# Kernel optimization log

Measured on AMD Instinct MI355X. Metric: run time of the kernel, lower is better.

The kernel has to match this reference:

```python
import jax, jax.numpy as jnp
import numpy as np

IN_FEATURES = 512
OUT_FEATURES = 512
B_EXP = 2.0
EPS = 1e-12  # torch F.normalize eps


def setup_inputs() -> dict:
    key = jax.random.key(0)
    kz, kw = jax.random.split(key)
    z = jax.random.normal(kz, (100000, IN_FEATURES), dtype=jnp.float32)
    weight = jax.random.normal(kw, (OUT_FEATURES, IN_FEATURES), dtype=jnp.float32) * (1.0 / np.sqrt(IN_FEATURES))
    return {"z": z, "weight": weight}


def reference(z, weight):
    # lin = z @ W^T : [N, out]
    lin = jnp.einsum('ni,oi->no', z, weight)
    # row-wise L2 normalize (torch F.normalize: x / max(||x||, eps))
    z_norm = z / jnp.maximum(jnp.linalg.norm(z, axis=1, keepdims=True), EPS)
    w_norm = weight / jnp.maximum(jnp.linalg.norm(weight, axis=1, keepdims=True), EPS)
    cos = jnp.einsum('ni,oi->no', z_norm, w_norm)
    scale = jnp.abs(cos) ** (B_EXP - 1.0)
    return lin * scale
```

## Files before the change

kernel.cpp:

```cpp
#include <hip/hip_runtime.h>
#include <hip/hip_bf16.h>
#include <stdint.h>


constexpr int KDIM = 512;
constexpr int NDIM = 512;

typedef __attribute__((ext_vector_type(8))) short bf16x8;
typedef __attribute__((ext_vector_type(4))) float f32x4;
typedef __attribute__((ext_vector_type(4))) uint32_t u32x4;

__device__ __forceinline__ uint32_t pk_bf16(float a, float b) {
  __hip_bfloat162 h = __float22bfloat162_rn(make_float2(a, b));
  union { __hip_bfloat162 h2; uint32_t u; } c;
  c.h2 = h;
  return c.u;
}

__device__ __forceinline__ void gload_lds16(const void* g, void* lds) {
  __builtin_amdgcn_global_load_lds(
      (const __attribute__((address_space(1))) uint32_t*)(uintptr_t)g,
      (__attribute__((address_space(3))) uint32_t*)(uintptr_t)lds,
      16, 0, 0);
}

__global__ __launch_bounds__(128) void prep_w(const float* __restrict__ w,
                                              unsigned short* __restrict__ wb,
                                              float* __restrict__ cninv) {
  const int row = blockIdx.x;
  const int t   = threadIdx.x;
  const float* gp = w + (size_t)row * KDIM + t * 4;
  f32x4 v = *(const f32x4*)gp;
  float s = v.x * v.x + v.y * v.y + v.z * v.z + v.w * v.w;

  uint2 p;
  p.x = pk_bf16(v.x, v.y);
  p.y = pk_bf16(v.z, v.w);
  *(uint2*)(wb + (size_t)row * KDIM + t * 4) = p;

  #pragma unroll
  for (int off = 32; off > 0; off >>= 1) s += __shfl_down(s, off, 64);
  __shared__ float red[2];
  if ((t & 63) == 0) red[t >> 6] = s;
  __syncthreads();
  if (t == 0) cninv[row] = 1.0f / fmaxf(sqrtf(red[0] + red[1]), 1e-12f);
}

__global__ __launch_bounds__(256) void gemm_bcos(const float* __restrict__ z,
                                                 const unsigned short* __restrict__ wb,
                                                 const float* __restrict__ cninv,
                                                 float* __restrict__ out, int M) {
  __shared__ unsigned short As[128 * 64];
  __shared__ unsigned short Bs[128 * 64];
  __shared__ float rowsq[128];
  __shared__ float rinv[128];

  const int t    = threadIdx.x;
  const int nb   = blockIdx.x;
  const int mb   = blockIdx.y;
  const int w    = t >> 6;
  const int lane = t & 63;
  const int lrow = lane & 15;
  const int quad = lane >> 4;
  const int wm   = (w & 1) * 64;
  const int wn   = (w >> 1) * 64;

  if (t < 128) rowsq[t] = 0.0f;

  f32x4 acc[4][4];
  #pragma unroll
  for (int i = 0; i < 4; ++i)
    #pragma unroll
    for (int j = 0; j < 4; ++j) acc[i][j] = (f32x4)0.0f;

  int rr[4];
  size_t gbase[4];
  #pragma unroll
  for (int i = 0; i < 4; ++i) {
    int gidx = t + 256 * i;
    rr[i] = gidx >> 3;
    int g = gidx & 7;
    int grow = mb * 128 + rr[i];
    if (grow >= M) grow = M - 1;
    gbase[i] = (size_t)grow * KDIM + g * 8;
  }

  float sq[4] = {0.f, 0.f, 0.f, 0.f};

  for (int kk = 0; kk < 8; ++kk) {
    const int kbase = kk * 64;
    __syncthreads();

    #pragma unroll
    for (int i = 0; i < 4; ++i) {
      int cidx = t + 256 * i;
      int r = cidx >> 3, c = cidx & 7;
      gload_lds16(wb + ((size_t)(nb * 128 + r) * KDIM + kbase + c * 8), &Bs[cidx * 8]);
    }

    #pragma unroll
    for (int i = 0; i < 4; ++i) {
      const float* gp = z + gbase[i] + kbase;
      f32x4 v0 = *(const f32x4*)gp;
      f32x4 v1 = *(const f32x4*)(gp + 4);
      sq[i] += v0.x * v0.x + v0.y * v0.y + v0.z * v0.z + v0.w * v0.w +
               v1.x * v1.x + v1.y * v1.y + v1.z * v1.z + v1.w * v1.w;
      u32x4 p;
      p.x = pk_bf16(v0.x, v0.y);
      p.y = pk_bf16(v0.z, v0.w);
      p.z = pk_bf16(v1.x, v1.y);
      p.w = pk_bf16(v1.z, v1.w);
      *(u32x4*)&As[(t + 256 * i) * 8] = p;
    }

    __syncthreads();

    #pragma unroll
    for (int ks = 0; ks < 2; ++ks) {
      const int k0 = ks * 32 + quad * 8;
      bf16x8 a[4], b[4];
      #pragma unroll
      for (int x = 0; x < 4; ++x) {
        a[x] = *(const bf16x8*)&As[(wm + x * 16 + lrow) * 64 + k0];
        b[x] = *(const bf16x8*)&Bs[(wn + x * 16 + lrow) * 64 + k0];
      }
      #pragma unroll
      for (int mt = 0; mt < 4; ++mt)
        #pragma unroll
        for (int nt = 0; nt < 4; ++nt)
          acc[mt][nt] = __builtin_amdgcn_mfma_f32_16x16x32_bf16(a[mt], b[nt], acc[mt][nt], 0, 0, 0);
    }
  }

  #pragma unroll
  for (int i = 0; i < 4; ++i) atomicAdd(&rowsq[rr[i]], sq[i]);
  __syncthreads();
  if (t < 128) rinv[t] = 1.0f / fmaxf(sqrtf(rowsq[t]), 1e-12f);
  __syncthreads();

  #pragma unroll
  for (int nt = 0; nt < 4; ++nt) {
    const int colg = nb * 128 + wn + nt * 16 + lrow;
    const float cv = cninv[colg];
    #pragma unroll
    for (int mt = 0; mt < 4; ++mt) {
      const int lrm = wm + mt * 16 + quad * 4;
      #pragma unroll
      for (int i = 0; i < 4; ++i) {
        const int rowg = mb * 128 + lrm + i;
        if (rowg < M) {
          const float v = acc[mt][nt][i];
          out[(size_t)rowg * NDIM + colg] = v * fabsf(v) * rinv[lrm + i] * cv;
        }
      }
    }
  }
}

extern "C" void kernel_launch(void* const* d_in, const int* in_sizes, int n_in,
                              void* d_out, int out_size, void* d_ws, size_t ws_size,
                              hipStream_t stream) {
  const float* z = (const float*)d_in[0];
  const float* w = (const float*)d_in[1];
  float* out = (float*)d_out;
  const int M = in_sizes[0] / KDIM;

  unsigned short* wb = (unsigned short*)d_ws;
  float* cninv = (float*)((char*)d_ws + (size_t)NDIM * KDIM * 2);

  prep_w<<<dim3(NDIM), dim3(128), 0, stream>>>(w, wb, cninv);

  dim3 grid(NDIM / 128, (M + 127) / 128);
  gemm_bcos<<<grid, dim3(256), 0, stream>>>(z, wb, cninv, out, M);
}
```

Measured before the change: 489.3 us.

## Restructure GEMM so each block owns full output rows with resident z tile

Each 512-thread block now loads a 64-row slab of z once, converts it to bf16 into an XOR-swizzled LDS tile covering the full K, and computes the row norms up front. Every wave then covers 64 output columns across all 512 columns, reading bf16 weights straight from global/L2 with no LDS staging and no per-K-step barriers. This removes the previous 4x re-read and re-conversion of z across column blocks. It also adds nontemporal loads and stores for streaming data. The cost is more L2 traffic for the weights and a 64KB LDS footprint that limits occupancy.

```diff
diff --git a/kernel.cpp b/kernel.cpp
--- a/kernel.cpp
+++ b/kernel.cpp
@@ -8,20 +8,12 @@
 
 typedef __attribute__((ext_vector_type(8))) short bf16x8;
 typedef __attribute__((ext_vector_type(4))) float f32x4;
-typedef __attribute__((ext_vector_type(4))) uint32_t u32x4;
 
 __device__ __forceinline__ uint32_t pk_bf16(float a, float b) {
   __hip_bfloat162 h = __float22bfloat162_rn(make_float2(a, b));
   union { __hip_bfloat162 h2; uint32_t u; } c;
   c.h2 = h;
   return c.u;
-}
-
-__device__ __forceinline__ void gload_lds16(const void* g, void* lds) {
-  __builtin_amdgcn_global_load_lds(
-      (const __attribute__((address_space(1))) uint32_t*)(uintptr_t)g,
-      (__attribute__((address_space(3))) uint32_t*)(uintptr_t)lds,
-      16, 0, 0);
 }
 
 __global__ __launch_bounds__(128) void prep_w(const float* __restrict__ w,
@@ -46,26 +38,46 @@
   if (t == 0) cninv[row] = 1.0f / fmaxf(sqrtf(red[0] + red[1]), 1e-12f);
 }
 
-__global__ __launch_bounds__(256) void gemm_bcos(const float* __restrict__ z,
-                                                 const unsigned short* __restrict__ wb,
-                                                 const float* __restrict__ cninv,
-                                                 float* __restrict__ out, int M) {
-  __shared__ unsigned short As[128 * 64];
-  __shared__ unsigned short Bs[128 * 64];
-  __shared__ float rowsq[128];
-  __shared__ float rinv[128];
+__global__ __launch_bounds__(512, 4) void gemm_bcos(const float* __restrict__ z,
+                                                    const unsigned short* __restrict__ wb,
+                                                    const float* __restrict__ cninv,
+                                                    float* __restrict__ out, int M) {
+  __shared__ unsigned short As[64 * 512];
+  __shared__ float rowsq[64];
+  __shared__ float rinv[64];
 
   const int t    = threadIdx.x;
-  const int nb   = blockIdx.x;
-  const int mb   = blockIdx.y;
   const int w    = t >> 6;
   const int lane = t & 63;
   const int lrow = lane & 15;
   const int quad = lane >> 4;
-  const int wm   = (w & 1) * 64;
-  const int wn   = (w >> 1) * 64;
+  const int mb   = blockIdx.x;
+  const int wn   = w * 64;
 
-  if (t < 128) rowsq[t] = 0.0f;
+  #pragma unroll
+  for (int rr = 0; rr < 8; ++rr) {
+    const int rl = w * 8 + rr;
+    int rg = mb * 64 + rl;
+    if (rg >= M) rg = M - 1;
+    const float* zp = z + (size_t)rg * KDIM;
+    float s = 0.0f;
+    #pragma unroll
+    for (int j = 0; j < 2; ++j) {
+      f32x4 v = __builtin_nontemporal_load((const f32x4*)(zp + j * 256 + lane * 4));
+      s += v.x * v.x + v.y * v.y + v.z * v.z + v.w * v.w;
+      uint2 p;
+      p.x = pk_bf16(v.x, v.y);
+      p.y = pk_bf16(v.z, v.w);
+      const int cb = (j * 512 + lane * 8) ^ (rr << 4);
+      *(uint2*)((char*)As + rl * 1024 + cb) = p;
+    }
+    #pragma unroll
+    for (int off = 32; off > 0; off >>= 1) s += __shfl_down(s, off, 64);
+    if (lane == 0) rowsq[rl] = s;
+  }
+  __syncthreads();
+  if (t < 64) rinv[t] = 1.0f / fmaxf(sqrtf(rowsq[t]), 1e-12f);
+  __syncthreads();
 
   f32x4 acc[4][4];
   #pragma unroll
@@ -73,84 +85,39 @@
     #pragma unroll
     for (int j = 0; j < 4; ++j) acc[i][j] = (f32x4)0.0f;
 
-  int rr[4];
-  size_t gbase[4];
-  #pragma unroll
-  for (int i = 0; i < 4; ++i) {
-    int gidx = t + 256 * i;
-    rr[i] = gidx >> 3;
-    int g = gidx & 7;
-    int grow = mb * 128 + rr[i];
-    if (grow >= M) grow = M - 1;
-    gbase[i] = (size_t)grow * KDIM + g * 8;
-  }
+  const int qs = (quad * 16) ^ ((lrow & 7) << 4);
+  const unsigned short* wbp = wb + (size_t)(wn + lrow) * KDIM + quad * 8;
 
-  float sq[4] = {0.f, 0.f, 0.f, 0.f};
-
-  for (int kk = 0; kk < 8; ++kk) {
-    const int kbase = kk * 64;
-    __syncthreads();
-
+  #pragma unroll 2
+  for (int ks = 0; ks < 16; ++ks) {
+    bf16x8 a[4], b[4];
     #pragma unroll
-    for (int i = 0; i < 4; ++i) {
-      int cidx = t + 256 * i;
-      int r = cidx >> 3, c = cidx & 7;
-      gload_lds16(wb + ((size_t)(nb * 128 + r) * KDIM + kbase + c * 8), &Bs[cidx * 8]);
-    }
-
+    for (int nt = 0; nt < 4; ++nt)
+      b[nt] = *(const bf16x8*)(wbp + nt * 16 * KDIM + ks * 32);
     #pragma unroll
-    for (int i = 0; i < 4; ++i) {
-      const float* gp = z + gbase[i] + kbase;
-      f32x4 v0 = *(const f32x4*)gp;
-      f32x4 v1 = *(const f32x4*)(gp + 4);
-      sq[i] += v0.x * v0.x + v0.y * v0.y + v0.z * v0.z + v0.w * v0.w +
-               v1.x * v1.x + v1.y * v1.y + v1.z * v1.z + v1.w * v1.w;
-      u32x4 p;
-      p.x = pk_bf16(v0.x, v0.y);
-      p.y = pk_bf16(v0.z, v0.w);
-      p.z = pk_bf16(v1.x, v1.y);
-      p.w = pk_bf16(v1.z, v1.w);
-      *(u32x4*)&As[(t + 256 * i) * 8] = p;
-    }
-
-    __syncthreads();
-
+    for (int mt = 0; mt < 4; ++mt)
+      a[mt] = *(const bf16x8*)((const char*)As + ((mt * 16 + lrow) << 10) + ((ks * 64) ^ qs));
     #pragma unroll
-    for (int ks = 0; ks < 2; ++ks) {
-      const int k0 = ks * 32 + quad * 8;
-      bf16x8 a[4], b[4];
+    for (int mt = 0; mt < 4; ++mt)
       #pragma unroll
-      for (int x = 0; x < 4; ++x) {
-        a[x] = *(const bf16x8*)&As[(wm + x * 16 + lrow) * 64 + k0];
-        b[x] = *(const bf16x8*)&Bs[(wn + x * 16 + lrow) * 64 + k0];
-      }
-      #pragma unroll
-      for (int mt = 0; mt < 4; ++mt)
-        #pragma unroll
-        for (int nt = 0; nt < 4; ++nt)
-          acc[mt][nt] = __builtin_amdgcn_mfma_f32_16x16x32_bf16(a[mt], b[nt], acc[mt][nt], 0, 0, 0);
-    }
+      for (int nt = 0; nt < 4; ++nt)
+        acc[mt][nt] = __builtin_amdgcn_mfma_f32_16x16x32_bf16(a[mt], b[nt], acc[mt][nt], 0, 0, 0);
   }
 
   #pragma unroll
-  for (int i = 0; i < 4; ++i) atomicAdd(&rowsq[rr[i]], sq[i]);
-  __syncthreads();
-  if (t < 128) rinv[t] = 1.0f / fmaxf(sqrtf(rowsq[t]), 1e-12f);
-  __syncthreads();
-
-  #pragma unroll
   for (int nt = 0; nt < 4; ++nt) {
-    const int colg = nb * 128 + wn + nt * 16 + lrow;
+    const int colg = wn + nt * 16 + lrow;
     const float cv = cninv[colg];
     #pragma unroll
     for (int mt = 0; mt < 4; ++mt) {
-      const int lrm = wm + mt * 16 + quad * 4;
+      const int rl = mt * 16 + quad * 4;
       #pragma unroll
       for (int i = 0; i < 4; ++i) {
-        const int rowg = mb * 128 + lrm + i;
+        const int rowg = mb * 64 + rl + i;
         if (rowg < M) {
           const float v = acc[mt][nt][i];
-          out[(size_t)rowg * NDIM + colg] = v * fabsf(v) * rinv[lrm + i] * cv;
+          __builtin_nontemporal_store(v * fabsf(v) * rinv[rl + i] * cv,
+                                      &out[(size_t)rowg * NDIM + colg]);
         }
       }
     }
@@ -170,6 +137,6 @@
 
   prep_w<<<dim3(NDIM), dim3(128), 0, stream>>>(w, wb, cninv);
 
-  dim3 grid(NDIM / 128, (M + 127) / 128);
-  gemm_bcos<<<grid, dim3(256), 0, stream>>>(z, wb, cninv, out, M);
+  dim3 grid((M + 63) / 64);
+  gemm_bcos<<<grid, dim3(512), 0, stream>>>(z, wb, cninv, out, M);
 }
```

Result: faster. 444.8 us (-9.1%).
